# Kernel optimization log

Hardware: AMD Instinct MI355X
Metric: run time of the kernel (lower is better)

## Reference

```python
import jax, jax.numpy as jnp
import numpy as np

N = 300000
H = 700
W_GRID = 700
CIN = 64
COUT = 64
K = 9


def setup_inputs() -> dict:
    rng = np.random.default_rng(0)
    lin = rng.permutation(H * W_GRID)[:N]
    ys = (lin // W_GRID).astype(np.int64)
    xs = (lin % W_GRID).astype(np.int64)
    grid = np.full(H * W_GRID, -1, np.int32)
    grid[lin] = np.arange(N, dtype=np.int32)
    offs = [(dy, dx) for dy in (-1, 0, 1) for dx in (-1, 0, 1)]

    def build(d):
        nbr = np.full((K, N), -1, np.int32)
        for k, (dy, dx) in enumerate(offs):
            ny = ys + dy * d
            nx = xs + dx * d
            valid = (ny >= 0) & (ny < H) & (nx >= 0) & (nx < W_GRID)
            l = np.clip(ny * W_GRID + nx, 0, H * W_GRID - 1)
            nbr[k] = np.where(valid, grid[l], -1)
        return jnp.asarray(nbr)

    nbr_d1 = build(1)
    nbr_d2 = build(2)

    key = jax.random.key(0)
    ks = jax.random.split(key, 16)
    f32 = jnp.float32

    def bn(k, c):
        s = jax.random.uniform(k, (c,), f32, 0.5, 1.5)
        b = jax.random.normal(jax.random.fold_in(k, 1), (c,), f32) * 0.1
        return s, b

    features = jax.random.normal(ks[0], (N, CIN), f32)
    W1 = jax.random.normal(ks[1], (K, CIN, COUT), f32) * 0.05
    W2a = jax.random.normal(ks[2], (CIN, COUT // 2), f32) * 0.05
    W2b = jax.random.normal(ks[3], (K, COUT // 2, COUT), f32) * 0.05
    W3 = jax.random.normal(ks[4], (K, CIN, COUT), f32) * 0.05
    Wf = jax.random.normal(ks[5], (3 * COUT, COUT), f32) * 0.05
    A1_w = jax.random.normal(ks[6], (3 * COUT, COUT // 4), f32) * 0.1
    A1_b = jnp.zeros((COUT // 4,), f32)
    A2_w = jax.random.normal(ks[7], (COUT // 4, 3 * COUT), f32) * 0.1
    A2_b = jnp.zeros((3 * COUT,), f32)
    bn1_s, bn1_b = bn(ks[8], COUT)
    bn2a_s, bn2a_b = bn(ks[9], COUT // 2)
    bn2b_s, bn2b_b = bn(ks[10], COUT)
    bn3_s, bn3_b = bn(ks[11], COUT)
    bnf_s, bnf_b = bn(ks[12], COUT)

    return dict(features=features, W1=W1, bn1_s=bn1_s, bn1_b=bn1_b,
                W2a=W2a, bn2a_s=bn2a_s, bn2a_b=bn2a_b,
                W2b=W2b, bn2b_s=bn2b_s, bn2b_b=bn2b_b,
                W3=W3, bn3_s=bn3_s, bn3_b=bn3_b,
                A1_w=A1_w, A1_b=A1_b, A2_w=A2_w, A2_b=A2_b,
                Wf=Wf, bnf_s=bnf_s, bnf_b=bnf_b,
                nbr_d1=nbr_d1, nbr_d2=nbr_d2)


def _sconv(f, nbr, W):
    # f: [N, Cin], nbr: [K, N] (-1 = no neighbor), W: [K, Cin, Cout]
    mask = (nbr >= 0)[..., None]                      # [K, N, 1]
    g = jnp.where(mask, f[jnp.clip(nbr, 0)], 0.0)     # [K, N, Cin] gather
    return jnp.einsum('knc,kcd->nd', g, W)            # [N, Cout]


def _bnrelu(x, s, b):
    # inference-mode BatchNorm folded into affine scale/shift, then ReLU
    return jax.nn.relu(x * s + b)


def reference(features, W1, bn1_s, bn1_b, W2a, bn2a_s, bn2a_b, W2b, bn2b_s, bn2b_b,
              W3, bn3_s, bn3_b, A1_w, A1_b, A2_w, A2_b, Wf, bnf_s, bnf_b,
              nbr_d1, nbr_d2):
    # path 1: 3x3 sparse conv + BN + ReLU
    feat1 = _bnrelu(_sconv(features, nbr_d1, W1), bn1_s, bn1_b)
    # path 2: 1x1 bottleneck + 3x3 sparse conv
    h = _bnrelu(features @ W2a, bn2a_s, bn2a_b)
    feat2 = _bnrelu(_sconv(h, nbr_d1, W2b), bn2b_s, bn2b_b)
    # path 3: 3x3 dilated (d=2) sparse conv
    feat3 = _bnrelu(_sconv(features, nbr_d2, W3), bn3_s, bn3_b)
    ms = jnp.concatenate([feat1, feat2, feat3], axis=1)   # [N, 3*Cout]
    # SE-style attention from global max pool over active sites
    pooled = jnp.max(ms, axis=0)                          # [3*Cout]
    attn = jax.nn.sigmoid(jax.nn.relu(pooled @ A1_w + A1_b) @ A2_w + A2_b)
    ms = ms * attn
    # 1x1 fusion conv + BN + ReLU
    fused = _bnrelu(ms @ Wf, bnf_s, bnf_b)                # [N, Cout]
    return fused
```

## Files before the change

### kernel.cpp

```cpp
#include <hip/hip_runtime.h>

#define N_PTS 300000
#define NPAD  300032
#define ZROW  N_PTS

typedef _Float16 f16;
typedef _Float16 f16x8 __attribute__((ext_vector_type(8)));
typedef float    f32x4 __attribute__((ext_vector_type(4)));

__device__ __forceinline__ f16 f2h(float x) { return (f16)x; }

union u4f16 { uint4 u; f16x8 h; };

#define HEAD_BLOCKS (NPAD / 256)
#define WP_BLOCKS   368

__global__ __launch_bounds__(256) void k_head(
    const float* __restrict__ feat, const float* __restrict__ W2a,
    const float* __restrict__ s2a, const float* __restrict__ b2a,
    const float* __restrict__ W1, const float* __restrict__ W2b,
    const float* __restrict__ W3,
    f16* __restrict__ featf, f16* __restrict__ hf,
    f16* __restrict__ Wt1, f16* __restrict__ Wt2b, f16* __restrict__ Wt3)
{
    if (blockIdx.x >= HEAD_BLOCKS) {
        int j = (blockIdx.x - HEAD_BLOCKS) * 256 + threadIdx.x;
        if (j < 36864) {
            int k = j >> 12, rem = j & 4095, d = rem >> 6, c = rem & 63;
            Wt1[j] = f2h(W1[(k << 12) + (c << 6) + d]);
        } else if (j < 73728) {
            int jj = j - 36864;
            int k = jj >> 12, rem = jj & 4095, d = rem >> 6, c = rem & 63;
            Wt3[jj] = f2h(W3[(k << 12) + (c << 6) + d]);
        } else if (j < 73728 + 18432) {
            int jj = j - 73728;
            int k = jj >> 11, rem = jj & 2047, d = rem >> 5, c2 = rem & 31;
            Wt2b[jj] = f2h(W2b[k * 2048 + c2 * 64 + d]);
        }
        return;
    }

    int lane = threadIdx.x & 63, wave = threadIdx.x >> 6;
    int n0 = (blockIdx.x * 4 + wave) * 64;
    int ln = lane & 15, q = lane >> 4;

    f16x8 a[4][2];
#pragma unroll
    for (int mt = 0; mt < 4; mt++) {
        int n = n0 + mt * 16 + ln;
#pragma unroll
        for (int ks = 0; ks < 2; ks++) {
            u4f16 v;
            if (n < N_PTS) {
                const float* p = feat + (long)n * 64 + ks * 32 + q * 8;
                float4 lo = *(const float4*)p;
                float4 hi = *(const float4*)(p + 4);
                v.h[0] = f2h(lo.x); v.h[1] = f2h(lo.y);
                v.h[2] = f2h(lo.z); v.h[3] = f2h(lo.w);
                v.h[4] = f2h(hi.x); v.h[5] = f2h(hi.y);
                v.h[6] = f2h(hi.z); v.h[7] = f2h(hi.w);
            } else {
                v.u = make_uint4(0u, 0u, 0u, 0u);
            }
            a[mt][ks] = v.h;
            *(uint4*)(featf + (long)n * 64 + ks * 32 + q * 8) = v.u;
        }
    }

    f32x4 acc[4][2];
    for (int mt = 0; mt < 4; mt++) for (int nt = 0; nt < 2; nt++)
        acc[mt][nt] = (f32x4){0.f, 0.f, 0.f, 0.f};
#pragma unroll
    for (int ks = 0; ks < 2; ks++)
#pragma unroll
        for (int nt = 0; nt < 2; nt++) {
            f16x8 b;
#pragma unroll
            for (int j = 0; j < 8; j++)
                b[j] = f2h(W2a[(ks * 32 + q * 8 + j) * 32 + nt * 16 + ln]);
#pragma unroll
            for (int mt = 0; mt < 4; mt++)
                acc[mt][nt] = __builtin_amdgcn_mfma_f32_16x16x32_f16(a[mt][ks], b, acc[mt][nt], 0, 0, 0);
        }

#pragma unroll
    for (int nt = 0; nt < 2; nt++) {
        int ch = nt * 16 + ln;
        float s = s2a[ch], bb = b2a[ch];
#pragma unroll
        for (int mt = 0; mt < 4; mt++)
#pragma unroll
            for (int r = 0; r < 4; r++) {
                int n = n0 + mt * 16 + q * 4 + r;
                float v = (n < N_PTS) ? fmaxf(acc[mt][nt][r] * s + bb, 0.f) : 0.f;
                hf[(long)n * 32 + ch] = f2h(v);
            }
    }
}

template <int CIN>
__device__ __forceinline__ void loadrows(
    uint4 (&dst)[4][CIN / 32], const int (&idx)[4],
    const f16* __restrict__ src, int q)
{
#pragma unroll
    for (int mt = 0; mt < 4; mt++) {
        const f16* p = src + (long)idx[mt] * CIN + q * 8;
#pragma unroll
        for (int ks = 0; ks < CIN / 32; ks++)
            dst[mt][ks] = *(const uint4*)(p + ks * 32);
    }
}

__device__ __forceinline__ void loadidx(
    int (&dst)[4], const int* __restrict__ nbr, int k, int n0, int ln)
{
    const int* nb = nbr + k * N_PTS;
#pragma unroll
    for (int mt = 0; mt < 4; mt++) {
        int nn = n0 + mt * 16 + ln;
        int v = (nn < N_PTS) ? nb[nn] : -1;
        dst[mt] = (v < 0) ? ZROW : v;
    }
}

template <int CIN>
__device__ __forceinline__ void conv_path(
    const f16* __restrict__ src, const f16* __restrict__ Wt,
    const int* __restrict__ nbr,
    int lane, int n0,
    const float* __restrict__ bns, const float* __restrict__ bnb,
    f16* __restrict__ msf, int colBase, float* __restrict__ pooled)
{
    constexpr int KS = CIN / 32;
    int ln = lane & 15, q = lane >> 4;

    f32x4 acc[4][4];
    for (int mt = 0; mt < 4; mt++) for (int nt = 0; nt < 4; nt++)
        acc[mt][nt] = (f32x4){0.f, 0.f, 0.f, 0.f};

    int  idxr[4][4];
    uint4 raw[4][4][KS];

#pragma unroll
    for (int k = 0; k < 4; k++) loadidx(idxr[k], nbr, k, n0, ln);
#pragma unroll
    for (int k = 0; k < 3; k++) loadrows<CIN>(raw[k], idxr[k], src, q);

#pragma unroll
    for (int k = 0; k < 9; k++) {
        if (k + 3 < 9) loadrows<CIN>(raw[(k + 3) & 3], idxr[(k + 3) & 3], src, q);
        if (k + 4 < 9) loadidx(idxr[k & 3], nbr, k + 4, n0, ln);
        const f16* Wk = Wt + k * CIN * 64;
#pragma unroll
        for (int ks = 0; ks < KS; ks++)
#pragma unroll
            for (int nt = 0; nt < 4; nt++) {
                f16x8 b = *(const f16x8*)(Wk + ((nt * 16 + ln) * CIN + ks * 32 + q * 8));
#pragma unroll
                for (int mt = 0; mt < 4; mt++) {
                    u4f16 v; v.u = raw[k & 3][mt][ks];
                    acc[mt][nt] = __builtin_amdgcn_mfma_f32_16x16x32_f16(v.h, b, acc[mt][nt], 0, 0, 0);
                }
            }
    }

#pragma unroll
    for (int nt = 0; nt < 4; nt++) {
        int ch = colBase + nt * 16 + ln;
        float s = bns[nt * 16 + ln], bb = bnb[nt * 16 + ln];
        float cmax = 0.f;
#pragma unroll
        for (int mt = 0; mt < 4; mt++)
#pragma unroll
            for (int r = 0; r < 4; r++) {
                int n = n0 + mt * 16 + q * 4 + r;
                float v = fmaxf(acc[mt][nt][r] * s + bb, 0.f);
                msf[(long)n * 192 + ch] = f2h(v);
                if (n < N_PTS) cmax = fmaxf(cmax, v);
            }
        cmax = fmaxf(cmax, __shfl_xor(cmax, 16));
        cmax = fmaxf(cmax, __shfl_xor(cmax, 32));
        if (q == 0) atomicMax((int*)(pooled + ch), __float_as_int(cmax));
    }
}

__global__ __launch_bounds__(256, 2) void k_conv(
    const f16* __restrict__ featf, const f16* __restrict__ hf,
    const f16* __restrict__ Wt1, const f16* __restrict__ Wt2b, const f16* __restrict__ Wt3,
    const int* __restrict__ nbr1, const int* __restrict__ nbr2,
    const float* __restrict__ bn1_s, const float* __restrict__ bn1_b,
    const float* __restrict__ bn2b_s, const float* __restrict__ bn2b_b,
    const float* __restrict__ bn3_s, const float* __restrict__ bn3_b,
    f16* __restrict__ msf, float* __restrict__ pooled)
{
    int lane = threadIdx.x & 63, wave = threadIdx.x >> 6;
    int u = blockIdx.x * 4 + wave;
    int tile = u / 3, path = u - tile * 3;
    int n0 = tile * 64;
    if (path == 0)
        conv_path<64>(featf, Wt1,  nbr1, lane, n0, bn1_s,  bn1_b,  msf, 0,   pooled);
    else if (path == 1)
        conv_path<32>(hf,    Wt2b, nbr1, lane, n0, bn2b_s, bn2b_b, msf, 64,  pooled);
    else
        conv_path<64>(featf, Wt3,  nbr2, lane, n0, bn3_s,  bn3_b,  msf, 128, pooled);
}

__global__ __launch_bounds__(256) void k_attn(
    const float* __restrict__ pooled,
    const float* __restrict__ A1w, const float* __restrict__ A1b,
    const float* __restrict__ A2w, const float* __restrict__ A2b,
    const float* __restrict__ Wf, f16* __restrict__ Wfst)
{
    __shared__ float sp[192], sa1[16], sattn[192];
    int t = threadIdx.x;
    if (t < 192) sp[t] = pooled[t];
    __syncthreads();
    if (t < 16) {
        float acc = A1b[t];
        for (int i = 0; i < 192; i++) acc += sp[i] * A1w[i * 16 + t];
        sa1[t] = fmaxf(acc, 0.f);
    }
    __syncthreads();
    if (t < 192) {
        float acc = A2b[t];
        for (int i = 0; i < 16; i++) acc += sa1[i] * A2w[i * 192 + t];
        sattn[t] = 1.f / (1.f + expf(-acc));
    }
    __syncthreads();
    for (int i = t; i < 192 * 64; i += 256) {
        int d = i / 192, j = i % 192;
        Wfst[i] = f2h(Wf[j * 64 + d] * sattn[j]);
    }
}

__global__ __launch_bounds__(256, 4) void k_fuse(
    const f16* __restrict__ msf, const f16* __restrict__ Wfst,
    const float* __restrict__ sf, const float* __restrict__ bf_,
    float* __restrict__ out)
{
    int lane = threadIdx.x & 63, wave = threadIdx.x >> 6;
    int n0 = (blockIdx.x * 4 + wave) * 32;
    int ln = lane & 15, q = lane >> 4;

    uint4 araw[6][2];
#pragma unroll
    for (int kt = 0; kt < 6; kt++)
#pragma unroll
        for (int mt = 0; mt < 2; mt++)
            araw[kt][mt] = *(const uint4*)(msf + (long)(n0 + mt * 16 + ln) * 192 + kt * 32 + q * 8);

    f32x4 acc[2][4];
    for (int mt = 0; mt < 2; mt++) for (int nt = 0; nt < 4; nt++)
        acc[mt][nt] = (f32x4){0.f, 0.f, 0.f, 0.f};

#pragma unroll
    for (int kt = 0; kt < 6; kt++)
#pragma unroll
        for (int nt = 0; nt < 4; nt++) {
            f16x8 b = *(const f16x8*)(Wfst + ((nt * 16 + ln) * 192 + kt * 32 + q * 8));
#pragma unroll
            for (int mt = 0; mt < 2; mt++) {
                u4f16 v; v.u = araw[kt][mt];
                acc[mt][nt] = __builtin_amdgcn_mfma_f32_16x16x32_f16(v.h, b, acc[mt][nt], 0, 0, 0);
            }
        }

#pragma unroll
    for (int nt = 0; nt < 4; nt++) {
        int ch = nt * 16 + ln;
        float s = sf[ch], bb = bf_[ch];
#pragma unroll
        for (int mt = 0; mt < 2; mt++)
#pragma unroll
            for (int r = 0; r < 4; r++) {
                int n = n0 + mt * 16 + q * 4 + r;
                if (n < N_PTS)
                    out[(long)n * 64 + ch] = fmaxf(acc[mt][nt][r] * s + bb, 0.f);
            }
    }
}

extern "C" void kernel_launch(void* const* d_in, const int* in_sizes, int n_in,
                              void* d_out, int out_size, void* d_ws, size_t ws_size,
                              hipStream_t stream)
{
    const float* features = (const float*)d_in[0];
    const float* W1     = (const float*)d_in[1];
    const float* bn1_s  = (const float*)d_in[2];
    const float* bn1_b  = (const float*)d_in[3];
    const float* W2a    = (const float*)d_in[4];
    const float* bn2a_s = (const float*)d_in[5];
    const float* bn2a_b = (const float*)d_in[6];
    const float* W2b    = (const float*)d_in[7];
    const float* bn2b_s = (const float*)d_in[8];
    const float* bn2b_b = (const float*)d_in[9];
    const float* W3     = (const float*)d_in[10];
    const float* bn3_s  = (const float*)d_in[11];
    const float* bn3_b  = (const float*)d_in[12];
    const float* A1w    = (const float*)d_in[13];
    const float* A1b    = (const float*)d_in[14];
    const float* A2w    = (const float*)d_in[15];
    const float* A2b    = (const float*)d_in[16];
    const float* Wf     = (const float*)d_in[17];
    const float* bnf_s  = (const float*)d_in[18];
    const float* bnf_b  = (const float*)d_in[19];
    const int*   nbr1   = (const int*)d_in[20];
    const int*   nbr2   = (const int*)d_in[21];

    char* ws = (char*)d_ws;
    size_t off = 0;
    f16* featf = (f16*)(ws + off); off += (size_t)NPAD * 64 * 2;
    f16* hf    = (f16*)(ws + off); off += (size_t)NPAD * 32 * 2;
    f16* msf   = (f16*)(ws + off); off += (size_t)NPAD * 192 * 2;
    f16* Wt1   = (f16*)(ws + off); off += 9 * 64 * 64 * 2;
    f16* Wt3   = (f16*)(ws + off); off += 9 * 64 * 64 * 2;
    f16* Wt2b  = (f16*)(ws + off); off += 9 * 32 * 64 * 2;
    f16* Wfst  = (f16*)(ws + off); off += 192 * 64 * 2;
    float* pooled = (float*)(ws + off); off += 256 * 4;

    hipMemsetAsync(pooled, 0, 192 * sizeof(float), stream);

    k_head<<<HEAD_BLOCKS + WP_BLOCKS, 256, 0, stream>>>(
        features, W2a, bn2a_s, bn2a_b, W1, W2b, W3,
        featf, hf, Wt1, Wt2b, Wt3);
    k_conv<<<(NPAD / 64) * 3 / 4, 256, 0, stream>>>(featf, hf, Wt1, Wt2b, Wt3, nbr1, nbr2,
                                           bn1_s, bn1_b, bn2b_s, bn2b_b, bn3_s, bn3_b,
                                           msf, pooled);
    k_attn<<<1, 256, 0, stream>>>(pooled, A1w, A1b, A2w, A2b, Wf, Wfst);
    k_fuse<<<NPAD / 128, 256, 0, stream>>>(msf, Wfst, bnf_s, bnf_b, (float*)d_out);
}
```

Baseline: 484.2 us.

## Stage per-path conv weights in LDS with lane-ordered fragment layout

Reorders the precomputed fp16 weight buffers (conv and fusion) so each MFMA B-fragment is a contiguous 512-element block indexed by lane, giving coalesced 16-byte loads. The conv kernel now assigns one path per block and copies that path's full weight set into shared memory before the gather-GEMM, so B operands come from LDS rather than global/L2. This adds a 72 KB LDS allocation per block plus a prologue copy and barrier, which may reduce occupancy below the requested two blocks per CU.

```diff
diff --git a/kernel.cpp b/kernel.cpp
--- a/kernel.cpp
+++ b/kernel.cpp
@@ -13,7 +13,8 @@
 union u4f16 { uint4 u; f16x8 h; };
 
 #define HEAD_BLOCKS (NPAD / 256)
-#define WP_BLOCKS   368
+#define WP_BLOCKS   360
+
 
 __global__ __launch_bounds__(256) void k_head(
     const float* __restrict__ feat, const float* __restrict__ W2a,
@@ -24,18 +25,23 @@
     f16* __restrict__ Wt1, f16* __restrict__ Wt2b, f16* __restrict__ Wt3)
 {
     if (blockIdx.x >= HEAD_BLOCKS) {
-        int j = (blockIdx.x - HEAD_BLOCKS) * 256 + threadIdx.x;
-        if (j < 36864) {
-            int k = j >> 12, rem = j & 4095, d = rem >> 6, c = rem & 63;
-            Wt1[j] = f2h(W1[(k << 12) + (c << 6) + d]);
-        } else if (j < 73728) {
-            int jj = j - 36864;
-            int k = jj >> 12, rem = jj & 4095, d = rem >> 6, c = rem & 63;
-            Wt3[jj] = f2h(W3[(k << 12) + (c << 6) + d]);
-        } else if (j < 73728 + 18432) {
-            int jj = j - 73728;
-            int k = jj >> 11, rem = jj & 2047, d = rem >> 5, c2 = rem & 31;
-            Wt2b[jj] = f2h(W2b[k * 2048 + c2 * 64 + d]);
+        int i = (blockIdx.x - HEAD_BLOCKS) * 256 + threadIdx.x;
+        if (i < 36864) {
+            int j = i & 7, lane = (i >> 3) & 63, nt = (i >> 9) & 3,
+                ks = (i >> 11) & 1, k = i >> 12;
+            int d = ks * 32 + (lane >> 4) * 8 + j, c = nt * 16 + (lane & 15);
+            Wt1[i] = f2h(W1[(k << 12) + (d << 6) + c]);
+        } else if (i < 73728) {
+            int ii = i - 36864;
+            int j = ii & 7, lane = (ii >> 3) & 63, nt = (ii >> 9) & 3,
+                ks = (ii >> 11) & 1, k = ii >> 12;
+            int d = ks * 32 + (lane >> 4) * 8 + j, c = nt * 16 + (lane & 15);
+            Wt3[ii] = f2h(W3[(k << 12) + (d << 6) + c]);
+        } else if (i < 92160) {
+            int ii = i - 73728;
+            int j = ii & 7, lane = (ii >> 3) & 63, nt = (ii >> 9) & 3, k = ii >> 11;
+            int d = (lane >> 4) * 8 + j, c = nt * 16 + (lane & 15);
+            Wt2b[ii] = f2h(W2b[k * 2048 + (d << 6) + c]);
         }
         return;
     }
@@ -126,7 +132,7 @@
 
 template <int CIN>
 __device__ __forceinline__ void conv_path(
-    const f16* __restrict__ src, const f16* __restrict__ Wt,
+    const f16* __restrict__ src, const f16* WtL,
     const int* __restrict__ nbr,
     int lane, int n0,
     const float* __restrict__ bns, const float* __restrict__ bnb,
@@ -151,12 +157,12 @@
     for (int k = 0; k < 9; k++) {
         if (k + 3 < 9) loadrows<CIN>(raw[(k + 3) & 3], idxr[(k + 3) & 3], src, q);
         if (k + 4 < 9) loadidx(idxr[k & 3], nbr, k + 4, n0, ln);
-        const f16* Wk = Wt + k * CIN * 64;
+        const f16* Wk = WtL + k * (KS * 4 * 512);
 #pragma unroll
         for (int ks = 0; ks < KS; ks++)
 #pragma unroll
             for (int nt = 0; nt < 4; nt++) {
-                f16x8 b = *(const f16x8*)(Wk + ((nt * 16 + ln) * CIN + ks * 32 + q * 8));
+                f16x8 b = *(const f16x8*)(Wk + (ks * 4 + nt) * 512 + lane * 8);
 #pragma unroll
                 for (int mt = 0; mt < 4; mt++) {
                     u4f16 v; v.u = raw[k & 3][mt][ks];
@@ -194,16 +200,25 @@
     const float* __restrict__ bn3_s, const float* __restrict__ bn3_b,
     f16* __restrict__ msf, float* __restrict__ pooled)
 {
+    __shared__ f16 smem[9 * 64 * 64];
+
+    int path = blockIdx.x % 3;
+    int g    = blockIdx.x / 3;
     int lane = threadIdx.x & 63, wave = threadIdx.x >> 6;
-    int u = blockIdx.x * 4 + wave;
-    int tile = u / 3, path = u - tile * 3;
-    int n0 = tile * 64;
+    int n0 = (g * 4 + wave) * 64;
+
+    const f16* Wsrc = (path == 0) ? Wt1 : (path == 1) ? Wt2b : Wt3;
+    int nchunk = (path == 1) ? (9 * 32 * 64 / 8) : (9 * 64 * 64 / 8);
+    for (int i = threadIdx.x; i < nchunk; i += 256)
+        ((uint4*)smem)[i] = ((const uint4*)Wsrc)[i];
+    __syncthreads();
+
     if (path == 0)
-        conv_path<64>(featf, Wt1,  nbr1, lane, n0, bn1_s,  bn1_b,  msf, 0,   pooled);
+        conv_path<64>(featf, smem, nbr1, lane, n0, bn1_s,  bn1_b,  msf, 0,   pooled);
     else if (path == 1)
-        conv_path<32>(hf,    Wt2b, nbr1, lane, n0, bn2b_s, bn2b_b, msf, 64,  pooled);
+        conv_path<32>(hf,    smem, nbr1, lane, n0, bn2b_s, bn2b_b, msf, 64,  pooled);
     else
-        conv_path<64>(featf, Wt3,  nbr2, lane, n0, bn3_s,  bn3_b,  msf, 128, pooled);
+        conv_path<64>(featf, smem, nbr2, lane, n0, bn3_s,  bn3_b,  msf, 128, pooled);
 }
 
 __global__ __launch_bounds__(256) void k_attn(
@@ -228,9 +243,10 @@
         sattn[t] = 1.f / (1.f + expf(-acc));
     }
     __syncthreads();
-    for (int i = t; i < 192 * 64; i += 256) {
-        int d = i / 192, j = i % 192;
-        Wfst[i] = f2h(Wf[j * 64 + d] * sattn[j]);
+    for (int i = t; i < 12288; i += 256) {
+        int j = i & 7, lane = (i >> 3) & 63, nt = (i >> 9) & 3, kt = i >> 11;
+        int jrow = kt * 32 + (lane >> 4) * 8 + j, c = nt * 16 + (lane & 15);
+        Wfst[i] = f2h(Wf[jrow * 64 + c] * sattn[jrow]);
     }
 }
 
@@ -258,7 +274,7 @@
     for (int kt = 0; kt < 6; kt++)
 #pragma unroll
         for (int nt = 0; nt < 4; nt++) {
-            f16x8 b = *(const f16x8*)(Wfst + ((nt * 16 + ln) * 192 + kt * 32 + q * 8));
+            f16x8 b = *(const f16x8*)(Wfst + ((kt * 4 + nt) * 64 + lane) * 8);
 #pragma unroll
             for (int mt = 0; mt < 2; mt++) {
                 u4f16 v; v.u = araw[kt][mt];
@@ -324,7 +340,7 @@
     k_head<<<HEAD_BLOCKS + WP_BLOCKS, 256, 0, stream>>>(
         features, W2a, bn2a_s, bn2a_b, W1, W2b, W3,
         featf, hf, Wt1, Wt2b, Wt3);
-    k_conv<<<(NPAD / 64) * 3 / 4, 256, 0, stream>>>(featf, hf, Wt1, Wt2b, Wt3, nbr1, nbr2,
+    k_conv<<<(NPAD / 64 / 4) * 3, 256, 0, stream>>>(featf, hf, Wt1, Wt2b, Wt3, nbr1, nbr2,
                                            bn1_s, bn1_b, bn2b_s, bn2b_b, bn3_s, bn3_b,
                                            msf, pooled);
     k_attn<<<1, 256, 0, stream>>>(pooled, A1w, A1b, A2w, A2b, Wf, Wfst);
```

After: 429.0 us. 11.4% less time.
